# Performance work log

Measured on AMD Instinct MI355X. Metric: run time of the kernel, lower is better.

The kernel has to match this reference:

```python
import jax, jax.numpy as jnp
import numpy as np

NS = 16384  # number of samples
N = 2048    # number of sites


def setup_inputs() -> dict:
    key = jax.random.key(0)
    kx, kk = jax.random.split(key)
    x = jax.random.normal(kx, (NS, N), dtype=jnp.float32)
    kernel = 0.01 * jax.random.normal(kk, (N * (N - 1) // 2,), dtype=jnp.float32)
    return {"x": x, "kernel": kernel, "n": 4}


def reference(x, kernel, n):
    # Build strictly lower-triangular W from the kernel vector (sorted, unique indices)
    Nloc = x.shape[-1]
    il = jnp.tril_indices(Nloc, k=-1)
    W = jnp.zeros((Nloc, Nloc), dtype=kernel.dtype).at[il].set(
        kernel, unique_indices=True, indices_are_sorted=True)
    # z_nj = sum_i x_ni W_ji  ==  x @ W.T
    z = x @ W.T
    # each step: z_nk = sum_j z_nj W_kj x_nj  ==  (z * x) @ W.T
    z = jax.lax.fori_loop(0, n - 2, lambda i, zz: (zz * x) @ W.T, z)
    # logpsi_n = sum_l z_nl x_nl
    return jnp.sum(z * x, axis=-1)
```

## Files before the change

### kernel.cpp

```cpp
#include <hip/hip_runtime.h>
#include <stdint.h>

#define NSAMP 16384
#define NSITE 2048
#define BM 128
#define BN 256
#define BK 32
#define NT_M (NSAMP / BM)
#define NT_N (NSITE / BN)

typedef _Float16 f16x8 __attribute__((ext_vector_type(8)));
typedef float f32x16 __attribute__((ext_vector_type(16)));

__device__ __forceinline__ unsigned short f2h(float f) {
  _Float16 h = (_Float16)f;
  return __builtin_bit_cast(unsigned short, h);
}
__device__ __forceinline__ float h2f(unsigned short u) {
  return (float)__builtin_bit_cast(_Float16, u);
}

__device__ __forceinline__ void gload_lds16(const void* g, void* l) {
  __builtin_amdgcn_global_load_lds(
      (const __attribute__((address_space(1))) void*)g,
      (__attribute__((address_space(3))) void*)l, 16, 0, 0);
}

#define SBAR() __builtin_amdgcn_sched_barrier(0)
#define BAR()  do { SBAR(); __builtin_amdgcn_s_barrier(); SBAR(); } while (0)
#define WLGKM(N) do { asm volatile("s_waitcnt lgkmcnt(" #N ")" ::: "memory"); SBAR(); } while (0)
#define WVM(N)   do { asm volatile("s_waitcnt vmcnt(" #N ")" ::: "memory"); SBAR(); } while (0)

__global__ void build_w_kernel(const float* __restrict__ kern,
                               unsigned short* __restrict__ W) {
  int idx = blockIdx.x * blockDim.x + threadIdx.x;
  int j = idx >> 11;
  int i = idx & (NSITE - 1);
  float v = 0.0f;
  if (i < j) v = kern[j * (j - 1) / 2 + i];
  W[idx] = f2h(v);
}

__global__ void build_x_kernel(const float* __restrict__ x,
                               unsigned short* __restrict__ X) {
  int idx = blockIdx.x * blockDim.x + threadIdx.x;
  const float4 v = reinterpret_cast<const float4*>(x)[idx];
  reinterpret_cast<ushort4*>(X)[idx] =
      make_ushort4(f2h(v.x), f2h(v.y), f2h(v.z), f2h(v.w));
}

template <int EPI>
__global__ __launch_bounds__(512, 4) void gemm_pass(
    const unsigned short* __restrict__ A, const unsigned short* __restrict__ W,
    const unsigned short* __restrict__ X, unsigned short* __restrict__ P,
    float* __restrict__ out) {
  __shared__ unsigned short lds[3][12288];

  const int bid = blockIdx.x;
  const int g = (bid >> 7) & 3;
  const int nt = (bid >> 9) ? (3 - g) : (7 - g);
  const int mt = bid & 127;
  const int m0 = mt * BM;
  const int n0 = nt * BN;

  const int tid = threadIdx.x;
  const int lane = tid & 63;
  const int wid = tid >> 6;
  const int wm = wid >> 2;
  const int wn = wid & 3;
  const int l32 = lane & 31;
  const int hi2 = lane >> 5;
  const int lbo = lane * 16;

  f32x16 acc[2][2] = {};

  const int nkt = 8 * (nt + 1);

  const int srow = ((tid >> 7) << 5) + (tid & 31);
  const int skk = (((tid >> 6) & 1) << 4) + (((tid >> 5) & 1) << 3);
  const unsigned short* sA = A + (size_t)(m0 + srow) * NSITE + skk;
  const unsigned short* sB0 = W + (size_t)(n0 + srow) * NSITE + skk;
  const unsigned short* sB1 = W + (size_t)(n0 + 128 + srow) * NSITE + skk;

  auto STAGE = [&](int kidx, int slot) {
    char* Ls = (char*)&lds[slot][0];
    const int ko = kidx * BK;
    gload_lds16(sA + ko, Ls + tid * 16);
    gload_lds16(sB0 + ko, Ls + 8192 + tid * 16);
    gload_lds16(sB1 + ko, Ls + 16384 + tid * 16);
  };

  STAGE(0, 0);
  STAGE(1, 1);
  WVM(3);
  BAR();

  int slot = 0, slot2 = 2;
  for (int t = 0; t < nkt; ++t) {
    const char* Ls = (const char*)&lds[slot][0];
    f16x8 a0, a1, b0, b1, a2, a3, b2, b3;
    a0 = *(const f16x8*)(Ls + (wm * 4 + 0) * 1024 + lbo);
    a1 = *(const f16x8*)(Ls + (wm * 4 + 2) * 1024 + lbo);
    b0 = *(const f16x8*)(Ls + 8192 + (wn * 4 + 0) * 1024 + lbo);
    b1 = *(const f16x8*)(Ls + 8192 + (wn * 4 + 2) * 1024 + lbo);
    SBAR();
    a2 = *(const f16x8*)(Ls + (wm * 4 + 1) * 1024 + lbo);
    a3 = *(const f16x8*)(Ls + (wm * 4 + 3) * 1024 + lbo);
    b2 = *(const f16x8*)(Ls + 8192 + (wn * 4 + 1) * 1024 + lbo);
    b3 = *(const f16x8*)(Ls + 8192 + (wn * 4 + 3) * 1024 + lbo);
    SBAR();
    if (t + 2 < nkt) STAGE(t + 2, slot2);
    WLGKM(4);
    __builtin_amdgcn_s_setprio(1);
    acc[0][0] = __builtin_amdgcn_mfma_f32_32x32x16_f16(a0, b0, acc[0][0], 0, 0, 0);
    acc[0][1] = __builtin_amdgcn_mfma_f32_32x32x16_f16(a0, b1, acc[0][1], 0, 0, 0);
    acc[1][0] = __builtin_amdgcn_mfma_f32_32x32x16_f16(a1, b0, acc[1][0], 0, 0, 0);
    acc[1][1] = __builtin_amdgcn_mfma_f32_32x32x16_f16(a1, b1, acc[1][1], 0, 0, 0);
    WLGKM(0);
    acc[0][0] = __builtin_amdgcn_mfma_f32_32x32x16_f16(a2, b2, acc[0][0], 0, 0, 0);
    acc[0][1] = __builtin_amdgcn_mfma_f32_32x32x16_f16(a2, b3, acc[0][1], 0, 0, 0);
    acc[1][0] = __builtin_amdgcn_mfma_f32_32x32x16_f16(a3, b2, acc[1][0], 0, 0, 0);
    acc[1][1] = __builtin_amdgcn_mfma_f32_32x32x16_f16(a3, b3, acc[1][1], 0, 0, 0);
    __builtin_amdgcn_s_setprio(0);
    if (t + 1 < nkt) {
      if (t + 2 < nkt) { WVM(3); } else { WVM(0); }
      BAR();
    }
    slot = (slot == 2) ? 0 : slot + 1;
    slot2 = (slot2 == 2) ? 0 : slot2 + 1;
  }

  if (EPI == 0) {
#pragma unroll
    for (int m = 0; m < 2; ++m)
#pragma unroll
      for (int n = 0; n < 2; ++n)
#pragma unroll
        for (int r = 0; r < 16; ++r) {
          const int row = (r & 3) + 8 * (r >> 2) + 4 * hi2;
          const int grow = m0 + wm * 64 + m * 32 + row;
          const int gcol = n0 + wn * 64 + n * 32 + l32;
          const size_t off = (size_t)grow * NSITE + gcol;
          P[off] = f2h(acc[m][n][r] * h2f(X[off]));
        }
  } else {
#pragma unroll
    for (int m = 0; m < 2; ++m)
#pragma unroll
      for (int r = 0; r < 16; ++r) {
        const int row = (r & 3) + 8 * (r >> 2) + 4 * hi2;
        const int grow = m0 + wm * 64 + m * 32 + row;
        const size_t base = (size_t)grow * NSITE + n0 + wn * 64 + l32;
        float s = acc[m][0][r] * h2f(X[base]) + acc[m][1][r] * h2f(X[base + 32]);
        s += __shfl_xor(s, 1);
        s += __shfl_xor(s, 2);
        s += __shfl_xor(s, 4);
        s += __shfl_xor(s, 8);
        s += __shfl_xor(s, 16);
        if (l32 == 0) atomicAdd(&out[grow], s);
      }
  }
}

extern "C" void kernel_launch(void* const* d_in, const int* in_sizes, int n_in,
                              void* d_out, int out_size, void* d_ws, size_t ws_size,
                              hipStream_t stream) {
  const float* x = (const float*)d_in[0];
  const float* kern = (const float*)d_in[1];
  float* out = (float*)d_out;

  unsigned short* W  = (unsigned short*)d_ws;
  unsigned short* X  = W + (size_t)NSITE * NSITE;
  unsigned short* P1 = X + (size_t)NSAMP * NSITE;
  unsigned short* P2 = P1 + (size_t)NSAMP * NSITE;

  hipMemsetAsync(d_out, 0, (size_t)NSAMP * sizeof(float), stream);
  build_w_kernel<<<(NSITE * NSITE) / 256, 256, 0, stream>>>(kern, W);
  build_x_kernel<<<(NSAMP * NSITE / 4) / 256, 256, 0, stream>>>(x, X);

  gemm_pass<0><<<NT_M * NT_N, 512, 0, stream>>>(X, W, X, P1, nullptr);
  gemm_pass<0><<<NT_M * NT_N, 512, 0, stream>>>(P1, W, X, P2, nullptr);
  gemm_pass<1><<<NT_M * NT_N, 512, 0, stream>>>(P2, W, X, nullptr, out);
}
```

Measured before the change: 408.3 us.

## Use 4-wave blocks with 64x128 per-wave tiles in GEMM passes

Shrinks each GEMM block from 8 waves to 4 waves over the same 128x256 tile, so every wave computes a 64x128 sub-tile with 2x4 MFMA accumulators instead of 2x2. Each thread now issues six global-to-LDS loads per stage instead of three, and the LDS fragment reads are reorganised, with the second half issued after the prefetch. The intent is to raise MFMA work per LDS read and cut barrier cost per block. In exchange it doubles accumulator register pressure and reduces the number of waves available to hide latency.

```diff
diff --git a/kernel.cpp b/kernel.cpp
--- a/kernel.cpp
+++ b/kernel.cpp
@@ -50,7 +50,7 @@
 }
 
 template <int EPI>
-__global__ __launch_bounds__(512, 4) void gemm_pass(
+__global__ __launch_bounds__(256, 2) void gemm_pass(
     const unsigned short* __restrict__ A, const unsigned short* __restrict__ W,
     const unsigned short* __restrict__ X, unsigned short* __restrict__ P,
     float* __restrict__ out) {
@@ -66,64 +66,81 @@
   const int tid = threadIdx.x;
   const int lane = tid & 63;
   const int wid = tid >> 6;
-  const int wm = wid >> 2;
-  const int wn = wid & 3;
+  const int wm = wid >> 1;
+  const int wn = wid & 1;
   const int l32 = lane & 31;
   const int hi2 = lane >> 5;
   const int lbo = lane * 16;
 
-  f32x16 acc[2][2] = {};
+  f32x16 acc[2][4] = {};
 
   const int nkt = 8 * (nt + 1);
 
-  const int srow = ((tid >> 7) << 5) + (tid & 31);
-  const int skk = (((tid >> 6) & 1) << 4) + (((tid >> 5) & 1) << 3);
-  const unsigned short* sA = A + (size_t)(m0 + srow) * NSITE + skk;
-  const unsigned short* sB0 = W + (size_t)(n0 + srow) * NSITE + skk;
-  const unsigned short* sB1 = W + (size_t)(n0 + 128 + srow) * NSITE + skk;
+  const int fsub = tid >> 6;
+  const int sl = tid & 63;
+  auto srcoff = [&](int f, int rbase) {
+    const int blk = f >> 1, s = f & 1;
+    return (size_t)(rbase + blk * 32 + (sl & 31)) * NSITE + s * 16 + (sl >> 5) * 8;
+  };
+  const unsigned short* sA0 = A + srcoff(fsub, m0);
+  const unsigned short* sA1 = A + srcoff(4 + fsub, m0);
+  const unsigned short* sB0 = W + srcoff(fsub, n0);
+  const unsigned short* sB1 = W + srcoff(4 + fsub, n0);
+  const unsigned short* sB2 = W + srcoff(8 + fsub, n0);
+  const unsigned short* sB3 = W + srcoff(12 + fsub, n0);
 
   auto STAGE = [&](int kidx, int slot) {
     char* Ls = (char*)&lds[slot][0];
     const int ko = kidx * BK;
-    gload_lds16(sA + ko, Ls + tid * 16);
+    gload_lds16(sA0 + ko, Ls + tid * 16);
+    gload_lds16(sA1 + ko, Ls + 4096 + tid * 16);
     gload_lds16(sB0 + ko, Ls + 8192 + tid * 16);
-    gload_lds16(sB1 + ko, Ls + 16384 + tid * 16);
+    gload_lds16(sB1 + ko, Ls + 12288 + tid * 16);
+    gload_lds16(sB2 + ko, Ls + 16384 + tid * 16);
+    gload_lds16(sB3 + ko, Ls + 20480 + tid * 16);
   };
 
   STAGE(0, 0);
   STAGE(1, 1);
-  WVM(3);
+  WVM(6);
   BAR();
 
   int slot = 0, slot2 = 2;
   for (int t = 0; t < nkt; ++t) {
     const char* Ls = (const char*)&lds[slot][0];
-    f16x8 a0, a1, b0, b1, a2, a3, b2, b3;
-    a0 = *(const f16x8*)(Ls + (wm * 4 + 0) * 1024 + lbo);
-    a1 = *(const f16x8*)(Ls + (wm * 4 + 2) * 1024 + lbo);
-    b0 = *(const f16x8*)(Ls + 8192 + (wn * 4 + 0) * 1024 + lbo);
-    b1 = *(const f16x8*)(Ls + 8192 + (wn * 4 + 2) * 1024 + lbo);
-    SBAR();
-    a2 = *(const f16x8*)(Ls + (wm * 4 + 1) * 1024 + lbo);
-    a3 = *(const f16x8*)(Ls + (wm * 4 + 3) * 1024 + lbo);
-    b2 = *(const f16x8*)(Ls + 8192 + (wn * 4 + 1) * 1024 + lbo);
-    b3 = *(const f16x8*)(Ls + 8192 + (wn * 4 + 3) * 1024 + lbo);
+    f16x8 fa[2][2], fb[2][4];
+#pragma unroll
+    for (int mb = 0; mb < 2; ++mb)
+      fa[0][mb] = *(const f16x8*)(Ls + ((wm * 2 + mb) * 2 + 0) * 1024 + lbo);
+#pragma unroll
+    for (int nb = 0; nb < 4; ++nb)
+      fb[0][nb] = *(const f16x8*)(Ls + 8192 + ((wn * 4 + nb) * 2 + 0) * 1024 + lbo);
     SBAR();
     if (t + 2 < nkt) STAGE(t + 2, slot2);
-    WLGKM(4);
+#pragma unroll
+    for (int mb = 0; mb < 2; ++mb)
+      fa[1][mb] = *(const f16x8*)(Ls + ((wm * 2 + mb) * 2 + 1) * 1024 + lbo);
+#pragma unroll
+    for (int nb = 0; nb < 4; ++nb)
+      fb[1][nb] = *(const f16x8*)(Ls + 8192 + ((wn * 4 + nb) * 2 + 1) * 1024 + lbo);
+    WLGKM(6);
     __builtin_amdgcn_s_setprio(1);
-    acc[0][0] = __builtin_amdgcn_mfma_f32_32x32x16_f16(a0, b0, acc[0][0], 0, 0, 0);
-    acc[0][1] = __builtin_amdgcn_mfma_f32_32x32x16_f16(a0, b1, acc[0][1], 0, 0, 0);
-    acc[1][0] = __builtin_amdgcn_mfma_f32_32x32x16_f16(a1, b0, acc[1][0], 0, 0, 0);
-    acc[1][1] = __builtin_amdgcn_mfma_f32_32x32x16_f16(a1, b1, acc[1][1], 0, 0, 0);
+#pragma unroll
+    for (int mb = 0; mb < 2; ++mb)
+#pragma unroll
+      for (int nb = 0; nb < 4; ++nb)
+        acc[mb][nb] = __builtin_amdgcn_mfma_f32_32x32x16_f16(fa[0][mb], fb[0][nb],
+                                                             acc[mb][nb], 0, 0, 0);
     WLGKM(0);
-    acc[0][0] = __builtin_amdgcn_mfma_f32_32x32x16_f16(a2, b2, acc[0][0], 0, 0, 0);
-    acc[0][1] = __builtin_amdgcn_mfma_f32_32x32x16_f16(a2, b3, acc[0][1], 0, 0, 0);
-    acc[1][0] = __builtin_amdgcn_mfma_f32_32x32x16_f16(a3, b2, acc[1][0], 0, 0, 0);
-    acc[1][1] = __builtin_amdgcn_mfma_f32_32x32x16_f16(a3, b3, acc[1][1], 0, 0, 0);
+#pragma unroll
+    for (int mb = 0; mb < 2; ++mb)
+#pragma unroll
+      for (int nb = 0; nb < 4; ++nb)
+        acc[mb][nb] = __builtin_amdgcn_mfma_f32_32x32x16_f16(fa[1][mb], fb[1][nb],
+                                                             acc[mb][nb], 0, 0, 0);
     __builtin_amdgcn_s_setprio(0);
     if (t + 1 < nkt) {
-      if (t + 2 < nkt) { WVM(3); } else { WVM(0); }
+      if (t + 2 < nkt) { WVM(6); } else { WVM(0); }
       BAR();
     }
     slot = (slot == 2) ? 0 : slot + 1;
@@ -134,12 +151,12 @@
 #pragma unroll
     for (int m = 0; m < 2; ++m)
 #pragma unroll
-      for (int n = 0; n < 2; ++n)
+      for (int n = 0; n < 4; ++n)
 #pragma unroll
         for (int r = 0; r < 16; ++r) {
           const int row = (r & 3) + 8 * (r >> 2) + 4 * hi2;
           const int grow = m0 + wm * 64 + m * 32 + row;
-          const int gcol = n0 + wn * 64 + n * 32 + l32;
+          const int gcol = n0 + wn * 128 + n * 32 + l32;
           const size_t off = (size_t)grow * NSITE + gcol;
           P[off] = f2h(acc[m][n][r] * h2f(X[off]));
         }
@@ -150,8 +167,9 @@
       for (int r = 0; r < 16; ++r) {
         const int row = (r & 3) + 8 * (r >> 2) + 4 * hi2;
         const int grow = m0 + wm * 64 + m * 32 + row;
-        const size_t base = (size_t)grow * NSITE + n0 + wn * 64 + l32;
-        float s = acc[m][0][r] * h2f(X[base]) + acc[m][1][r] * h2f(X[base + 32]);
+        const size_t base = (size_t)grow * NSITE + n0 + wn * 128 + l32;
+        float s = acc[m][0][r] * h2f(X[base]) + acc[m][1][r] * h2f(X[base + 32]) +
+                  acc[m][2][r] * h2f(X[base + 64]) + acc[m][3][r] * h2f(X[base + 96]);
         s += __shfl_xor(s, 1);
         s += __shfl_xor(s, 2);
         s += __shfl_xor(s, 4);
@@ -178,7 +196,7 @@
   build_w_kernel<<<(NSITE * NSITE) / 256, 256, 0, stream>>>(kern, W);
   build_x_kernel<<<(NSAMP * NSITE / 4) / 256, 256, 0, stream>>>(x, X);
 
-  gemm_pass<0><<<NT_M * NT_N, 512, 0, stream>>>(X, W, X, P1, nullptr);
-  gemm_pass<0><<<NT_M * NT_N, 512, 0, stream>>>(P1, W, X, P2, nullptr);
-  gemm_pass<1><<<NT_M * NT_N, 512, 0, stream>>>(P2, W, X, nullptr, out);
-}
+  gemm_pass<0><<<NT_M * NT_N, 256, 0, stream>>>(X, W, X, P1, nullptr);
+  gemm_pass<0><<<NT_M * NT_N, 256, 0, stream>>>(P1, W, X, P2, nullptr);
+  gemm_pass<1><<<NT_M * NT_N, 256, 0, stream>>>(P2, W, X, nullptr, out);
+}
```

Result: slower. 416.5 us (+2.0%).

## Pre-pack operands into MFMA fragment layout and load W directly to registers

Applied to the files above, without the earlier changes.

The operand matrices W, X and the intermediate products are now stored in a pre-packed fragment layout, so each 32x16 fragment is a contiguous 1 KB chunk. W fragments are loaded straight from global memory into registers with a one-step prefetch instead of going through LDS. The M tile grows to 256 rows, giving each wave 4x2 accumulators and more MFMA work per LDS read. The epilogue writes packed P through LDS. The trade-offs are higher register pressure, which drops launch bounds occupancy from 4 to 2, an extra row-major X copy in workspace, and B operands fetched from global memory with latency that LDS no longer hides.

```diff
diff --git a/kernel.cpp b/kernel.cpp
--- a/kernel.cpp
+++ b/kernel.cpp
@@ -3,7 +3,7 @@
 
 #define NSAMP 16384
 #define NSITE 2048
-#define BM 128
+#define BM 256
 #define BN 256
 #define BK 32
 #define NT_M (NSAMP / BM)
@@ -31,127 +31,180 @@
 #define WLGKM(N) do { asm volatile("s_waitcnt lgkmcnt(" #N ")" ::: "memory"); SBAR(); } while (0)
 #define WVM(N)   do { asm volatile("s_waitcnt vmcnt(" #N ")" ::: "memory"); SBAR(); } while (0)
 
+
 __global__ void build_w_kernel(const float* __restrict__ kern,
-                               unsigned short* __restrict__ W) {
-  int idx = blockIdx.x * blockDim.x + threadIdx.x;
-  int j = idx >> 11;
-  int i = idx & (NSITE - 1);
-  float v = 0.0f;
-  if (i < j) v = kern[j * (j - 1) / 2 + i];
-  W[idx] = f2h(v);
+                               unsigned short* __restrict__ Wp) {
+  const int idx = blockIdx.x * blockDim.x + threadIdx.x;
+  const int lane = idx & 63;
+  const int kb = (idx >> 6) & 127;
+  const int rbG = idx >> 13;
+  const int j = rbG * 32 + (lane & 31);
+  const int i0 = kb * 16 + (lane >> 5) * 8;
+  const long long tri = (long long)j * (j - 1) / 2;
+  unsigned short v[8];
+#pragma unroll
+  for (int e = 0; e < 8; ++e) {
+    const int i = i0 + e;
+    float f = (i < j) ? kern[tri + i] : 0.0f;
+    v[e] = f2h(f);
+  }
+  ushort4* dst = (ushort4*)(Wp + (size_t)idx * 8);
+  dst[0] = make_ushort4(v[0], v[1], v[2], v[3]);
+  dst[1] = make_ushort4(v[4], v[5], v[6], v[7]);
 }
 
 __global__ void build_x_kernel(const float* __restrict__ x,
-                               unsigned short* __restrict__ X) {
-  int idx = blockIdx.x * blockDim.x + threadIdx.x;
-  const float4 v = reinterpret_cast<const float4*>(x)[idx];
-  reinterpret_cast<ushort4*>(X)[idx] =
-      make_ushort4(f2h(v.x), f2h(v.y), f2h(v.z), f2h(v.w));
+                               unsigned short* __restrict__ Xp,
+                               unsigned short* __restrict__ Xrow) {
+  const int idx = blockIdx.x * blockDim.x + threadIdx.x;
+  const int row = idx >> 8;
+  const int c8 = idx & 255;
+  const float4 v0 = ((const float4*)x)[(size_t)idx * 2];
+  const float4 v1 = ((const float4*)x)[(size_t)idx * 2 + 1];
+  const ushort4 h0 = make_ushort4(f2h(v0.x), f2h(v0.y), f2h(v0.z), f2h(v0.w));
+  const ushort4 h1 = make_ushort4(f2h(v1.x), f2h(v1.y), f2h(v1.z), f2h(v1.w));
+  ushort4* dr = (ushort4*)(Xrow + (size_t)idx * 8);
+  dr[0] = h0;
+  dr[1] = h1;
+  const int rbG = row >> 5, kb = c8 >> 1;
+  const int lane = (c8 & 1) * 32 + (row & 31);
+  ushort4* dp = (ushort4*)(Xp + (((size_t)rbG * 128 + kb) * 64 + lane) * 8);
+  dp[0] = h0;
+  dp[1] = h1;
 }
 
 template <int EPI>
-__global__ __launch_bounds__(512, 4) void gemm_pass(
-    const unsigned short* __restrict__ A, const unsigned short* __restrict__ W,
-    const unsigned short* __restrict__ X, unsigned short* __restrict__ P,
+__global__ __launch_bounds__(512, 2) void gemm_pass(
+    const unsigned short* __restrict__ Ap, const unsigned short* __restrict__ Wp,
+    const unsigned short* __restrict__ Xrow, unsigned short* __restrict__ Pp,
     float* __restrict__ out) {
-  __shared__ unsigned short lds[3][12288];
+  __shared__ unsigned short lds[3 * 8192];
 
   const int bid = blockIdx.x;
-  const int g = (bid >> 7) & 3;
-  const int nt = (bid >> 9) ? (3 - g) : (7 - g);
-  const int mt = bid & 127;
-  const int m0 = mt * BM;
-  const int n0 = nt * BN;
-
-  const int tid = threadIdx.x;
-  const int lane = tid & 63;
-  const int wid = tid >> 6;
+  const int cohort = (bid >> 6) & 3;
+  const int nt = (bid >> 8) ? cohort : (7 - cohort);
+  const int mt = bid & 63;
+  const int m0 = mt * BM, n0 = nt * BN;
+
+  const int tid = threadIdx.x, lane = tid & 63, wid = tid >> 6;
   const int wm = wid >> 2;
   const int wn = wid & 3;
-  const int l32 = lane & 31;
-  const int hi2 = lane >> 5;
-  const int lbo = lane * 16;
-
-  f32x16 acc[2][2] = {};
-
+  const int l32 = lane & 31, hi2 = lane >> 5;
   const int nkt = 8 * (nt + 1);
 
-  const int srow = ((tid >> 7) << 5) + (tid & 31);
-  const int skk = (((tid >> 6) & 1) << 4) + (((tid >> 5) & 1) << 3);
-  const unsigned short* sA = A + (size_t)(m0 + srow) * NSITE + skk;
-  const unsigned short* sB0 = W + (size_t)(n0 + srow) * NSITE + skk;
-  const unsigned short* sB1 = W + (size_t)(n0 + 128 + srow) * NSITE + skk;
-
-  auto STAGE = [&](int kidx, int slot) {
-    char* Ls = (char*)&lds[slot][0];
-    const int ko = kidx * BK;
-    gload_lds16(sA + ko, Ls + tid * 16);
-    gload_lds16(sB0 + ko, Ls + 8192 + tid * 16);
-    gload_lds16(sB1 + ko, Ls + 16384 + tid * 16);
+  f32x16 acc[4][2] = {};
+
+  const int rbG0 = m0 >> 5;
+  const int fi0 = wid, fi1 = 8 + wid;
+  const unsigned short* srcA0 =
+      Ap + (((size_t)(rbG0 + (fi0 >> 1)) * 128 + (fi0 & 1)) * 64 + lane) * 8;
+  const unsigned short* srcA1 =
+      Ap + (((size_t)(rbG0 + (fi1 >> 1)) * 128 + (fi1 & 1)) * 64 + lane) * 8;
+  const int dA0 = fi0 * 1024 + lane * 16;
+  const int dA1 = fi1 * 1024 + lane * 16;
+  auto STAGE = [&](int kidx, int slotbase) {
+    gload_lds16(srcA0 + (size_t)kidx * 1024, (char*)lds + slotbase + dA0);
+    gload_lds16(srcA1 + (size_t)kidx * 1024, (char*)lds + slotbase + dA1);
   };
 
-  STAGE(0, 0);
-  STAGE(1, 1);
-  WVM(3);
+  const int cbG = nt * 8 + wn * 2;
+  const unsigned short* wp00 = Wp + (((size_t)(cbG + 0) * 128 + 0) * 64 + lane) * 8;
+  const unsigned short* wp01 = Wp + (((size_t)(cbG + 0) * 128 + 1) * 64 + lane) * 8;
+  const unsigned short* wp10 = Wp + (((size_t)(cbG + 1) * 128 + 0) * 64 + lane) * 8;
+  const unsigned short* wp11 = Wp + (((size_t)(cbG + 1) * 128 + 1) * 64 + lane) * 8;
+
+  int sl0 = 0, sl1 = 16384, sl2 = 32768;
+
+  STAGE(0, sl0);
+  SBAR();
+  f16x8 b00 = *(const f16x8*)(wp00);
+  f16x8 b01 = *(const f16x8*)(wp01);
+  f16x8 b10 = *(const f16x8*)(wp10);
+  f16x8 b11 = *(const f16x8*)(wp11);
+  SBAR();
+  STAGE(1, sl1);
+  WVM(2);
   BAR();
 
-  int slot = 0, slot2 = 2;
   for (int t = 0; t < nkt; ++t) {
-    const char* Ls = (const char*)&lds[slot][0];
-    f16x8 a0, a1, b0, b1, a2, a3, b2, b3;
-    a0 = *(const f16x8*)(Ls + (wm * 4 + 0) * 1024 + lbo);
-    a1 = *(const f16x8*)(Ls + (wm * 4 + 2) * 1024 + lbo);
-    b0 = *(const f16x8*)(Ls + 8192 + (wn * 4 + 0) * 1024 + lbo);
-    b1 = *(const f16x8*)(Ls + 8192 + (wn * 4 + 2) * 1024 + lbo);
+    f16x8 fa0[4], fa1[4];
+#pragma unroll
+    for (int mb = 0; mb < 4; ++mb)
+      fa0[mb] = *(const f16x8*)((char*)lds + sl0 + ((wm * 4 + mb) * 2 + 0) * 1024 + lane * 16);
+#pragma unroll
+    for (int mb = 0; mb < 4; ++mb)
+      fa1[mb] = *(const f16x8*)((char*)lds + sl0 + ((wm * 4 + mb) * 2 + 1) * 1024 + lane * 16);
     SBAR();
-    a2 = *(const f16x8*)(Ls + (wm * 4 + 1) * 1024 + lbo);
-    a3 = *(const f16x8*)(Ls + (wm * 4 + 3) * 1024 + lbo);
-    b2 = *(const f16x8*)(Ls + 8192 + (wn * 4 + 1) * 1024 + lbo);
-    b3 = *(const f16x8*)(Ls + 8192 + (wn * 4 + 3) * 1024 + lbo);
+    const bool hasB = (t + 1 < nkt);
+    f16x8 n00, n01, n10, n11;
+    if (hasB) {
+      n00 = *(const f16x8*)(wp00 + (size_t)(t + 1) * 1024);
+      n01 = *(const f16x8*)(wp01 + (size_t)(t + 1) * 1024);
+      n10 = *(const f16x8*)(wp10 + (size_t)(t + 1) * 1024);
+      n11 = *(const f16x8*)(wp11 + (size_t)(t + 1) * 1024);
+    }
     SBAR();
-    if (t + 2 < nkt) STAGE(t + 2, slot2);
+    if (t + 2 < nkt) STAGE(t + 2, sl2);
     WLGKM(4);
     __builtin_amdgcn_s_setprio(1);
-    acc[0][0] = __builtin_amdgcn_mfma_f32_32x32x16_f16(a0, b0, acc[0][0], 0, 0, 0);
-    acc[0][1] = __builtin_amdgcn_mfma_f32_32x32x16_f16(a0, b1, acc[0][1], 0, 0, 0);
-    acc[1][0] = __builtin_amdgcn_mfma_f32_32x32x16_f16(a1, b0, acc[1][0], 0, 0, 0);
-    acc[1][1] = __builtin_amdgcn_mfma_f32_32x32x16_f16(a1, b1, acc[1][1], 0, 0, 0);
+#pragma unroll
+    for (int mb = 0; mb < 4; ++mb) {
+      acc[mb][0] = __builtin_amdgcn_mfma_f32_32x32x16_f16(fa0[mb], b00, acc[mb][0], 0, 0, 0);
+      acc[mb][1] = __builtin_amdgcn_mfma_f32_32x32x16_f16(fa0[mb], b10, acc[mb][1], 0, 0, 0);
+    }
     WLGKM(0);
-    acc[0][0] = __builtin_amdgcn_mfma_f32_32x32x16_f16(a2, b2, acc[0][0], 0, 0, 0);
-    acc[0][1] = __builtin_amdgcn_mfma_f32_32x32x16_f16(a2, b3, acc[0][1], 0, 0, 0);
-    acc[1][0] = __builtin_amdgcn_mfma_f32_32x32x16_f16(a3, b2, acc[1][0], 0, 0, 0);
-    acc[1][1] = __builtin_amdgcn_mfma_f32_32x32x16_f16(a3, b3, acc[1][1], 0, 0, 0);
+#pragma unroll
+    for (int mb = 0; mb < 4; ++mb) {
+      acc[mb][0] = __builtin_amdgcn_mfma_f32_32x32x16_f16(fa1[mb], b01, acc[mb][0], 0, 0, 0);
+      acc[mb][1] = __builtin_amdgcn_mfma_f32_32x32x16_f16(fa1[mb], b11, acc[mb][1], 0, 0, 0);
+    }
     __builtin_amdgcn_s_setprio(0);
+    if (hasB) { b00 = n00; b01 = n01; b10 = n10; b11 = n11; }
     if (t + 1 < nkt) {
-      if (t + 2 < nkt) { WVM(3); } else { WVM(0); }
+      if (t + 2 < nkt) { WVM(2); } else { WVM(0); }
       BAR();
     }
-    slot = (slot == 2) ? 0 : slot + 1;
-    slot2 = (slot2 == 2) ? 0 : slot2 + 1;
+    const int tmp = sl0; sl0 = sl1; sl1 = sl2; sl2 = tmp;
   }
 
+  BAR();
+
+  const int ebase = wid * 4096;
   if (EPI == 0) {
 #pragma unroll
-    for (int m = 0; m < 2; ++m)
-#pragma unroll
-      for (int n = 0; n < 2; ++n)
+    for (int mb = 0; mb < 4; ++mb) {
+      const int growb = m0 + wm * 128 + mb * 32;
+#pragma unroll
+      for (int nb = 0; nb < 2; ++nb)
 #pragma unroll
         for (int r = 0; r < 16; ++r) {
           const int row = (r & 3) + 8 * (r >> 2) + 4 * hi2;
-          const int grow = m0 + wm * 64 + m * 32 + row;
-          const int gcol = n0 + wn * 64 + n * 32 + l32;
-          const size_t off = (size_t)grow * NSITE + gcol;
-          P[off] = f2h(acc[m][n][r] * h2f(X[off]));
+          const int col = nb * 32 + l32;
+          const unsigned short xv =
+              Xrow[(size_t)(growb + row) * NSITE + n0 + wn * 64 + col];
+          const unsigned short pv = f2h(acc[mb][nb][r] * h2f(xv));
+          *(volatile unsigned short*)((char*)lds + ebase + row * 128 + col * 2) = pv;
         }
+      WLGKM(0);
+      const int rbG = growb >> 5;
+#pragma unroll
+      for (int kbl = 0; kbl < 4; ++kbl) {
+        f16x8 fr = *(const f16x8*)((char*)lds + ebase + l32 * 128 + kbl * 32 + hi2 * 16);
+        const int kbG = ((n0 + wn * 64) >> 4) + kbl;
+        *(f16x8*)(Pp + (((size_t)rbG * 128 + kbG) * 64 + lane) * 8) = fr;
+      }
+      WLGKM(0);
+    }
   } else {
 #pragma unroll
-    for (int m = 0; m < 2; ++m)
+    for (int mb = 0; mb < 4; ++mb) {
+      const int growb = m0 + wm * 128 + mb * 32;
 #pragma unroll
       for (int r = 0; r < 16; ++r) {
         const int row = (r & 3) + 8 * (r >> 2) + 4 * hi2;
-        const int grow = m0 + wm * 64 + m * 32 + row;
-        const size_t base = (size_t)grow * NSITE + n0 + wn * 64 + l32;
-        float s = acc[m][0][r] * h2f(X[base]) + acc[m][1][r] * h2f(X[base + 32]);
+        const int grow = growb + row;
+        const size_t xb = (size_t)grow * NSITE + n0 + wn * 64 + l32;
+        float s = acc[mb][0][r] * h2f(Xrow[xb]) + acc[mb][1][r] * h2f(Xrow[xb + 32]);
         s += __shfl_xor(s, 1);
         s += __shfl_xor(s, 2);
         s += __shfl_xor(s, 4);
@@ -159,6 +212,7 @@
         s += __shfl_xor(s, 16);
         if (l32 == 0) atomicAdd(&out[grow], s);
       }
+    }
   }
 }
 
@@ -169,16 +223,17 @@
   const float* kern = (const float*)d_in[1];
   float* out = (float*)d_out;
 
-  unsigned short* W  = (unsigned short*)d_ws;
-  unsigned short* X  = W + (size_t)NSITE * NSITE;
-  unsigned short* P1 = X + (size_t)NSAMP * NSITE;
-  unsigned short* P2 = P1 + (size_t)NSAMP * NSITE;
+  unsigned short* Wp   = (unsigned short*)d_ws;
+  unsigned short* Xp   = Wp + (size_t)NSITE * NSITE;
+  unsigned short* Xrow = Xp + (size_t)NSAMP * NSITE;
+  unsigned short* P1   = Xrow + (size_t)NSAMP * NSITE;
+  unsigned short* P2   = P1 + (size_t)NSAMP * NSITE;
 
   hipMemsetAsync(d_out, 0, (size_t)NSAMP * sizeof(float), stream);
-  build_w_kernel<<<(NSITE * NSITE) / 256, 256, 0, stream>>>(kern, W);
-  build_x_kernel<<<(NSAMP * NSITE / 4) / 256, 256, 0, stream>>>(x, X);
-
-  gemm_pass<0><<<NT_M * NT_N, 512, 0, stream>>>(X, W, X, P1, nullptr);
-  gemm_pass<0><<<NT_M * NT_N, 512, 0, stream>>>(P1, W, X, P2, nullptr);
-  gemm_pass<1><<<NT_M * NT_N, 512, 0, stream>>>(P2, W, X, nullptr, out);
-}
+  build_w_kernel<<<(NSITE * NSITE / 8) / 256, 256, 0, stream>>>(kern, Wp);
+  build_x_kernel<<<(NSAMP * NSITE / 8) / 256, 256, 0, stream>>>(x, Xp, Xrow);
+
+  gemm_pass<0><<<NT_M * NT_N, 512, 0, stream>>>(Xp, Wp, Xrow, P1, nullptr);
+  gemm_pass<0><<<NT_M * NT_N, 512, 0, stream>>>(P1, Wp, Xrow, P2, nullptr);
+  gemm_pass<1><<<NT_M * NT_N, 512, 0, stream>>>(P2, Wp, Xrow, nullptr, out);
+}
```

Measured after the change: 553.9 us. 35.7% more time.
